# Optimization experiments

Measured on AMD Instinct MI355X. Metric: run time of the kernel, lower is better.

The kernel has to match this reference:

```python
import math
import jax, jax.numpy as jnp
import numpy as np

VMIN, VMAX = 0.0, 1.0
NUM_BINS = 64
SIGMA = 0.5 * (VMAX - VMIN) / NUM_BINS  # matches torch: sigma * (vmax-vmin)/num_bins
EPS = 1e-10


def setup_inputs() -> dict:
    key = jax.random.key(0)
    k1, k2 = jax.random.split(key)
    shape = (2, 1, 96, 96, 96)
    tar = jax.random.uniform(k1, shape, dtype=jnp.float32)
    src = jax.random.uniform(k2, shape, dtype=jnp.float32)
    return {"tar": tar, "src": src}


def _normalise_minmax(x, min_out, max_out):
    # x: (N, P) -- per-sample min-max normalisation to [min_out, max_out]
    xmin = jnp.min(x, axis=1, keepdims=True)
    xmax = jnp.max(x, axis=1, keepdims=True)
    return (x - xmin) / (xmax - xmin + EPS) * (max_out - min_out) + min_out


def _windowed(x, bins):
    # x: (N, P), bins: (B,) -> (N, B, P) Gaussian kernel weights
    d = x[:, None, :] - bins[None, :, None]
    return jnp.exp(-(d * d) / (2.0 * SIGMA * SIGMA)) / math.sqrt(2.0 * math.pi) * SIGMA


def reference(tar, src):
    N = tar.shape[0]
    # use channel 0 only, flatten spatial dims
    t = _normalise_minmax(tar[:, 0].reshape(N, -1), VMIN, VMAX)
    s = _normalise_minmax(src[:, 0].reshape(N, -1), VMIN, VMAX)

    bins = jnp.linspace(VMIN, VMAX, NUM_BINS, dtype=tar.dtype)
    w_tar = _windowed(t, bins)  # (N, B, P)
    w_src = _windowed(s, bins)  # (N, B, P)

    hist_joint = jnp.einsum('nbp,ncp->nbc', w_tar, w_src)  # (N, B, B)
    hist_norm = jnp.sum(hist_joint, axis=(1, 2), keepdims=True)
    p_joint = hist_joint / hist_norm

    p_tar = jnp.sum(p_joint, axis=2)  # (N, B)
    p_src = jnp.sum(p_joint, axis=1)  # (N, B)

    ent_tar = -jnp.sum(p_tar * jnp.log(p_tar + EPS), axis=1)
    ent_src = -jnp.sum(p_src * jnp.log(p_src + EPS), axis=1)
    ent_joint = -jnp.sum(p_joint * jnp.log(p_joint + EPS), axis=(1, 2))

    # normalised=True branch
    return -jnp.mean((ent_tar + ent_src) / ent_joint)
```

## Files before the change

### kernel.cpp

```cpp
#include <hip/hip_runtime.h>
#include <math.h>

#define NBINS 64
#define HIST_ELEMS (NBINS*NBINS)
#define PTS_PER_BLOCK 2304
#define GXN 384
#define CHUNKS 18
#define LSTRIDE 68
#define SQK 1.7256062f
#define SMEM_FLOATS (2*PTS_PER_BLOCK + NBINS*LSTRIDE)
#define RED_BLOCKS 128
#define TILES_PER_WAVE (GXN/4)

typedef float f4 __attribute__((ext_vector_type(4)));
typedef float f2 __attribute__((ext_vector_type(2)));
typedef float f32x4 __attribute__((ext_vector_type(4)));
typedef _Float16 half8 __attribute__((ext_vector_type(8)));
typedef int int4v __attribute__((ext_vector_type(4)));
typedef unsigned int u32x2 __attribute__((ext_vector_type(2)));

static __device__ __forceinline__ half8 pack8(const float* w) {
    int4v v;
    v[0] = __builtin_bit_cast(int, __builtin_amdgcn_cvt_pkrtz(w[0], w[1]));
    v[1] = __builtin_bit_cast(int, __builtin_amdgcn_cvt_pkrtz(w[2], w[3]));
    v[2] = __builtin_bit_cast(int, __builtin_amdgcn_cvt_pkrtz(w[4], w[5]));
    v[3] = __builtin_bit_cast(int, __builtin_amdgcn_cvt_pkrtz(w[6], w[7]));
    return __builtin_bit_cast(half8, v);
}

static __device__ __forceinline__ f2 pk_fma(f2 a, f2 b, f2 c) {
    f2 d;
    asm("v_pk_fma_f32 %0, %1, %2, %3" : "=v"(d) : "v"(a), "v"(b), "v"(c));
    return d;
}
static __device__ __forceinline__ f2 pk_mul(f2 a, f2 b) {
    f2 d;
    asm("v_pk_mul_f32 %0, %1, %2" : "=v"(d) : "v"(a), "v"(b));
    return d;
}

__global__ __launch_bounds__(256) void minmax_kernel(const float* __restrict__ tar,
                                                     const float* __restrict__ src,
                                                     float* __restrict__ pm,
                                                     unsigned* __restrict__ ctr,
                                                     float* __restrict__ hist, int P) {
    const int b = blockIdx.x, n = blockIdx.y, t = blockIdx.z;
    const f4* x = (const f4*)((t == 0 ? tar : src) + (size_t)n * P);
    const int per = (P / 4) / 64;
    float lmin = INFINITY, lmax = -INFINITY;
    for (int i = b * per + threadIdx.x; i < (b + 1) * per; i += 256) {
        f4 v = x[i];
        lmin = fminf(lmin, fminf(fminf(v[0], v[1]), fminf(v[2], v[3])));
        lmax = fmaxf(lmax, fmaxf(fmaxf(v[0], v[1]), fmaxf(v[2], v[3])));
    }
    for (int off = 32; off > 0; off >>= 1) {
        lmin = fminf(lmin, __shfl_down(lmin, off, 64));
        lmax = fmaxf(lmax, __shfl_down(lmax, off, 64));
    }
    __shared__ float smin[4], smax[4];
    const int lane = threadIdx.x & 63, wave = threadIdx.x >> 6;
    if (lane == 0) { smin[wave] = lmin; smax[wave] = lmax; }
    __syncthreads();
    if (threadIdx.x == 0) {
        pm[(n * 2 + t) * 64 + b] =
            fminf(fminf(smin[0], smin[1]), fminf(smin[2], smin[3]));
        pm[256 + (n * 2 + t) * 64 + b] =
            fmaxf(fmaxf(smax[0], smax[1]), fmaxf(smax[2], smax[3]));
    }
    const int flat = b + 64 * n + 128 * t;
    f4* hz = (f4*)hist + flat * 8;
    const f4 z = {0.f, 0.f, 0.f, 0.f};
    if (threadIdx.x < 8) hz[threadIdx.x] = z;
    if (flat == 0 && threadIdx.x == 0) *ctr = 0u;
}

template <int STAGED>
__global__ __launch_bounds__(256) void mfma_hist_kernel(const float* __restrict__ tar,
                                                        const float* __restrict__ src,
                                                        const float* __restrict__ pm,
                                                        _Float16* __restrict__ bh,
                                                        float* __restrict__ hist,
                                                        int P) {
    const int n = blockIdx.y;
    const int bx = blockIdx.x;
    const int tid = threadIdx.x;
    const int lane = tid & 63, wave = tid >> 6;
    const int mlane = lane & 15, quad = lane >> 4;

    __shared__ float smem[SMEM_FLOATS];
    __shared__ float mmred[4];
    float* su_t = smem;
    float* su_s = smem + PTS_PER_BLOCK;
    float* lh = smem + 2 * PTS_PER_BLOCK;

    if (wave == 0) {
        float a = pm[(n * 2 + 0) * 64 + lane];
        float b = pm[256 + (n * 2 + 0) * 64 + lane];
        float c = pm[(n * 2 + 1) * 64 + lane];
        float d = pm[256 + (n * 2 + 1) * 64 + lane];
        for (int off = 32; off > 0; off >>= 1) {
            a = fminf(a, __shfl_down(a, off, 64));
            b = fmaxf(b, __shfl_down(b, off, 64));
            c = fminf(c, __shfl_down(c, off, 64));
            d = fmaxf(d, __shfl_down(d, off, 64));
        }
        if (lane == 0) { mmred[0] = a; mmred[1] = b; mmred[2] = c; mmred[3] = d; }
    }

    {
        const f4* tg = (const f4*)(tar + (size_t)n * P + (size_t)bx * PTS_PER_BLOCK);
        const f4* sg = (const f4*)(src + (size_t)n * P + (size_t)bx * PTS_PER_BLOCK);
        f4* st4 = (f4*)su_t;
        f4* ss4 = (f4*)su_s;
        #pragma unroll
        for (int k = 0; k < 2; ++k) {
            const int i = tid + k * 256;
            st4[i] = tg[i];
            ss4[i] = sg[i];
        }
        if (tid < 64) {
            const int i = 512 + tid;
            st4[i] = tg[i];
            ss4[i] = sg[i];
        }
    }
    __syncthreads();

    const float tmin = mmred[0], tmax = mmred[1];
    const float smin = mmred[2], smax = mmred[3];
    const float tk = 63.0f / (tmax - tmin + 1e-10f) * SQK;
    const float sk = 63.0f / (smax - smin + 1e-10f) * SQK;
    const f2 tkk = {tk, tk}, skk = {sk, sk};
    f2 tneg[4], sneg[4];
    #pragma unroll
    for (int mt = 0; mt < 4; ++mt) {
        const float b = SQK * (float)(mlane + 16 * mt);
        const float tb_ = tmin * tk + b;
        const float sb_ = smin * sk + b;
        tneg[mt] = {-tb_, -tb_};
        sneg[mt] = {-sb_, -sb_};
    }

    f32x4 acc[4][4];
    #pragma unroll
    for (int a = 0; a < 4; ++a)
        #pragma unroll
        for (int b = 0; b < 4; ++b) acc[a][b] = (f32x4){0.f, 0.f, 0.f, 0.f};

    const int kwbase = wave * (32 * CHUNKS) + quad * 8;
    #pragma unroll 3
    for (int c = 0; c < CHUNKS; ++c) {
        const int kbase = kwbase + c * 32;
        const f4* pt4 = (const f4*)&su_t[kbase];
        const f4* ps4 = (const f4*)&su_s[kbase];
        f4 ta = pt4[0], tb = pt4[1];
        f4 sa = ps4[0], sb = ps4[1];
        f2 tp[4], sp[4];
        tp[0] = {ta[0], ta[1]}; tp[1] = {ta[2], ta[3]};
        tp[2] = {tb[0], tb[1]}; tp[3] = {tb[2], tb[3]};
        sp[0] = {sa[0], sa[1]}; sp[1] = {sa[2], sa[3]};
        sp[2] = {sb[0], sb[1]}; sp[3] = {sb[2], sb[3]};

        half8 af[4], bf[4];
        #pragma unroll
        for (int mt = 0; mt < 4; ++mt) {
            float w[8];
            #pragma unroll
            for (int h = 0; h < 4; ++h) {
                f2 d = pk_fma(tp[h], tkk, tneg[mt]);
                f2 s2 = pk_mul(d, d);
                w[2 * h]     = __builtin_amdgcn_exp2f(-s2[0]);
                w[2 * h + 1] = __builtin_amdgcn_exp2f(-s2[1]);
            }
            af[mt] = pack8(w);
        }
        #pragma unroll
        for (int nt = 0; nt < 4; ++nt) {
            float w[8];
            #pragma unroll
            for (int h = 0; h < 4; ++h) {
                f2 d = pk_fma(sp[h], skk, sneg[nt]);
                f2 s2 = pk_mul(d, d);
                w[2 * h]     = __builtin_amdgcn_exp2f(-s2[0]);
                w[2 * h + 1] = __builtin_amdgcn_exp2f(-s2[1]);
            }
            bf[nt] = pack8(w);
        }
        #pragma unroll
        for (int mt = 0; mt < 4; ++mt)
            #pragma unroll
            for (int nt = 0; nt < 4; ++nt)
                acc[mt][nt] = __builtin_amdgcn_mfma_f32_16x16x32_f16(
                    af[mt], bf[nt], acc[mt][nt], 0, 0, 0);
    }

    #pragma unroll
    for (int w = 0; w < 4; ++w) {
        if (wave == w) {
            #pragma unroll
            for (int nt = 0; nt < 4; ++nt)
                #pragma unroll
                for (int mt = 0; mt < 4; ++mt) {
                    f4* p = (f4*)&lh[(16 * nt + mlane) * LSTRIDE + 16 * mt + 4 * quad];
                    if (w == 0) {
                        *p = acc[mt][nt];
                    } else {
                        f4 v = *p;
                        v += acc[mt][nt];
                        *p = v;
                    }
                }
        }
        __syncthreads();
    }

    if (STAGED) {
        u32x2* dst = (u32x2*)(bh + ((size_t)n * GXN + bx) * HIST_ELEMS);
        #pragma unroll
        for (int k = 0; k < 4; ++k) {
            const int i4 = tid + k * 256;
            const int c = i4 >> 4, r4 = (i4 & 15) * 4;
            f4 v = *(const f4*)&lh[c * LSTRIDE + r4];
            u32x2 o;
            o[0] = __builtin_bit_cast(unsigned int, __builtin_amdgcn_cvt_pkrtz(v[0], v[1]));
            o[1] = __builtin_bit_cast(unsigned int, __builtin_amdgcn_cvt_pkrtz(v[2], v[3]));
            dst[i4] = o;
        }
    } else {
        float* gh = hist + (size_t)n * HIST_ELEMS;
        for (int i = tid; i < HIST_ELEMS; i += 256) {
            const int c = i >> 6, r = i & 63;
            unsafeAtomicAdd(&gh[i], lh[c * LSTRIDE + r]);
        }
    }
}

__global__ __launch_bounds__(256) void reduce_finalize_kernel(const _Float16* __restrict__ bh,
                                                              float* __restrict__ hist,
                                                              unsigned* __restrict__ ctr,
                                                              float* __restrict__ out,
                                                              int staged) {
    const int tid = threadIdx.x;
    const int lane = tid & 63, wave = tid >> 6;
    __shared__ float h2[2 * HIST_ELEMS];
    __shared__ float buf[4], rowsum[NBINS], colsum[NBINS], colp[4 * NBINS];
    __shared__ float part[4][64];
    __shared__ int lastflag;

    if (staged) {
        const int g = blockIdx.x * 64 + lane;
        const int n = g >> 12, e = g & 4095;
        const _Float16* p = bh + (((size_t)(n * GXN + wave * TILES_PER_WAVE)) << 12) + e;
        float s = 0.0f;
        #pragma unroll 8
        for (int b = 0; b < TILES_PER_WAVE; ++b) s += (float)p[(size_t)b << 12];
        part[wave][lane] = s;
        __syncthreads();
        if (wave == 0)
            hist[g] = part[0][lane] + part[1][lane] + part[2][lane] + part[3][lane];
    }

    __threadfence();
    if (tid == 0) {
        unsigned old = atomicAdd(ctr, 1u);
        lastflag = (old == RED_BLOCKS - 1) ? 1 : 0;
    }
    __syncthreads();
    if (!lastflag) return;

    for (int i = tid; i < 2 * HIST_ELEMS; i += 256)
        h2[i] = __hip_atomic_load(&hist[i], __ATOMIC_RELAXED, __HIP_MEMORY_SCOPE_SYSTEM);
    __syncthreads();

    float accl = 0.0f;
    for (int nn = 0; nn < 2; ++nn) {
        const float* h = h2 + nn * HIST_ELEMS;
        {
            int r = tid >> 2, q = tid & 3;
            const float* hp = h + r * NBINS + q * 16;
            float sv = 0.0f;
            #pragma unroll
            for (int k = 0; k < 16; ++k) sv += hp[k];
            sv += __shfl_down(sv, 1, 64);
            sv += __shfl_down(sv, 2, 64);
            if (q == 0) rowsum[r] = sv;
        }
        {
            int c = tid & 63, g = tid >> 6;
            const float* hp = h + (g * 16) * NBINS + c;
            float sv = 0.0f;
            #pragma unroll
            for (int k = 0; k < 16; ++k) sv += hp[k * NBINS];
            colp[g * NBINS + c] = sv;
        }
        __syncthreads();
        if (tid < NBINS)
            colsum[tid] = colp[0 * NBINS + tid] + colp[1 * NBINS + tid] +
                          colp[2 * NBINS + tid] + colp[3 * NBINS + tid];
        __syncthreads();

        float tv = (tid < NBINS) ? rowsum[tid] : 0.0f;
        for (int off = 32; off > 0; off >>= 1) tv += __shfl_down(tv, off, 64);
        __syncthreads();
        if (lane == 0) buf[wave] = tv;
        __syncthreads();
        const float total = buf[0] + buf[1] + buf[2] + buf[3];
        const float inv = 1.0f / total;

        float ej = 0.0f;
        for (int i = tid; i < HIST_ELEMS; i += 256) {
            float p = h[i] * inv;
            ej += p * __logf(p + 1e-10f);
        }
        for (int off = 32; off > 0; off >>= 1) ej += __shfl_down(ej, off, 64);
        __syncthreads();
        if (lane == 0) buf[wave] = ej;
        __syncthreads();
        const float entj = -(buf[0] + buf[1] + buf[2] + buf[3]);

        float em = 0.0f;
        if (tid < NBINS) {
            float p = rowsum[tid] * inv;
            em = p * __logf(p + 1e-10f);
        } else if (tid < 2 * NBINS) {
            float p = colsum[tid - NBINS] * inv;
            em = p * __logf(p + 1e-10f);
        }
        for (int off = 32; off > 0; off >>= 1) em += __shfl_down(em, off, 64);
        __syncthreads();
        if (lane == 0) buf[wave] = em;
        __syncthreads();
        const float ents = -(buf[0] + buf[1] + buf[2] + buf[3]);

        accl += ents / entj;
        __syncthreads();
    }
    if (tid == 0) out[0] = -0.5f * accl;
}

extern "C" void kernel_launch(void* const* d_in, const int* in_sizes, int n_in,
                              void* d_out, int out_size, void* d_ws, size_t ws_size,
                              hipStream_t stream) {
    const float* tar = (const float*)d_in[0];
    const float* src = (const float*)d_in[1];
    const int N = 2;
    const int P = in_sizes[0] / N;

    float* pm = (float*)d_ws;
    unsigned* ctr = (unsigned*)((char*)d_ws + 2048);
    float* hist = (float*)((char*)d_ws + 4096);
    _Float16* bh = (_Float16*)((char*)d_ws + 36864);
    float* out = (float*)d_out;

    const size_t need = 36864 + (size_t)2 * GXN * HIST_ELEMS * sizeof(_Float16);

    minmax_kernel<<<dim3(64, N, 2), 256, 0, stream>>>(tar, src, pm, ctr, hist, P);
    if (ws_size >= need) {
        mfma_hist_kernel<1><<<dim3(GXN, N), 256, 0, stream>>>(tar, src, pm, bh, hist, P);
        reduce_finalize_kernel<<<RED_BLOCKS, 256, 0, stream>>>(bh, hist, ctr, out, 1);
    } else {
        mfma_hist_kernel<0><<<dim3(GXN, N), 256, 0, stream>>>(tar, src, pm, bh, hist, P);
        reduce_finalize_kernel<<<RED_BLOCKS, 256, 0, stream>>>(bh, hist, ctr, out, 0);
    }
}
```

Baseline: 129.2 us.

## Halve points per block, drop LDS staging, and widen reduction reads

```diff
diff --git a/kernel.cpp b/kernel.cpp
--- a/kernel.cpp
+++ b/kernel.cpp
@@ -3,14 +3,13 @@
 
 #define NBINS 64
 #define HIST_ELEMS (NBINS*NBINS)
-#define PTS_PER_BLOCK 2304
-#define GXN 384
-#define CHUNKS 18
+#define PTS_PER_BLOCK 1152
+#define GXN 768
+#define CHUNKS 9
 #define LSTRIDE 68
 #define SQK 1.7256062f
-#define SMEM_FLOATS (2*PTS_PER_BLOCK + NBINS*LSTRIDE)
+#define MMB 128
 #define RED_BLOCKS 128
-#define TILES_PER_WAVE (GXN/4)
 
 typedef float f4 __attribute__((ext_vector_type(4)));
 typedef float f2 __attribute__((ext_vector_type(2)));
@@ -46,7 +45,7 @@
                                                      float* __restrict__ hist, int P) {
     const int b = blockIdx.x, n = blockIdx.y, t = blockIdx.z;
     const f4* x = (const f4*)((t == 0 ? tar : src) + (size_t)n * P);
-    const int per = (P / 4) / 64;
+    const int per = (P / 4) / MMB;
     float lmin = INFINITY, lmax = -INFINITY;
     for (int i = b * per + threadIdx.x; i < (b + 1) * per; i += 256) {
         f4 v = x[i];
@@ -62,42 +61,41 @@
     if (lane == 0) { smin[wave] = lmin; smax[wave] = lmax; }
     __syncthreads();
     if (threadIdx.x == 0) {
-        pm[(n * 2 + t) * 64 + b] =
+        pm[(n * 2 + t) * MMB + b] =
             fminf(fminf(smin[0], smin[1]), fminf(smin[2], smin[3]));
-        pm[256 + (n * 2 + t) * 64 + b] =
+        pm[512 + (n * 2 + t) * MMB + b] =
             fmaxf(fmaxf(smax[0], smax[1]), fmaxf(smax[2], smax[3]));
     }
-    const int flat = b + 64 * n + 128 * t;
-    f4* hz = (f4*)hist + flat * 8;
+    const int flat = b + MMB * (n * 2 + t);
+    f4* hz = (f4*)hist + flat * 4;
     const f4 z = {0.f, 0.f, 0.f, 0.f};
-    if (threadIdx.x < 8) hz[threadIdx.x] = z;
+    if (threadIdx.x < 4) hz[threadIdx.x] = z;
     if (flat == 0 && threadIdx.x == 0) *ctr = 0u;
 }
 
 template <int STAGED>
-__global__ __launch_bounds__(256) void mfma_hist_kernel(const float* __restrict__ tar,
-                                                        const float* __restrict__ src,
-                                                        const float* __restrict__ pm,
-                                                        _Float16* __restrict__ bh,
-                                                        float* __restrict__ hist,
-                                                        int P) {
+__global__ __launch_bounds__(256, 6) void mfma_hist_kernel(const float* __restrict__ tar,
+                                                           const float* __restrict__ src,
+                                                           const float* __restrict__ pm,
+                                                           _Float16* __restrict__ bh,
+                                                           float* __restrict__ hist,
+                                                           int P) {
     const int n = blockIdx.y;
     const int bx = blockIdx.x;
     const int tid = threadIdx.x;
     const int lane = tid & 63, wave = tid >> 6;
     const int mlane = lane & 15, quad = lane >> 4;
 
-    __shared__ float smem[SMEM_FLOATS];
+    __shared__ float lh[NBINS * LSTRIDE];
     __shared__ float mmred[4];
-    float* su_t = smem;
-    float* su_s = smem + PTS_PER_BLOCK;
-    float* lh = smem + 2 * PTS_PER_BLOCK;
 
     if (wave == 0) {
-        float a = pm[(n * 2 + 0) * 64 + lane];
-        float b = pm[256 + (n * 2 + 0) * 64 + lane];
-        float c = pm[(n * 2 + 1) * 64 + lane];
-        float d = pm[256 + (n * 2 + 1) * 64 + lane];
+        float a = fminf(pm[(n * 2 + 0) * MMB + lane], pm[(n * 2 + 0) * MMB + 64 + lane]);
+        float b = fmaxf(pm[512 + (n * 2 + 0) * MMB + lane],
+                        pm[512 + (n * 2 + 0) * MMB + 64 + lane]);
+        float c = fminf(pm[(n * 2 + 1) * MMB + lane], pm[(n * 2 + 1) * MMB + 64 + lane]);
+        float d = fmaxf(pm[512 + (n * 2 + 1) * MMB + lane],
+                        pm[512 + (n * 2 + 1) * MMB + 64 + lane]);
         for (int off = 32; off > 0; off >>= 1) {
             a = fminf(a, __shfl_down(a, off, 64));
             b = fmaxf(b, __shfl_down(b, off, 64));
@@ -105,24 +103,6 @@
             d = fmaxf(d, __shfl_down(d, off, 64));
         }
         if (lane == 0) { mmred[0] = a; mmred[1] = b; mmred[2] = c; mmred[3] = d; }
-    }
-
-    {
-        const f4* tg = (const f4*)(tar + (size_t)n * P + (size_t)bx * PTS_PER_BLOCK);
-        const f4* sg = (const f4*)(src + (size_t)n * P + (size_t)bx * PTS_PER_BLOCK);
-        f4* st4 = (f4*)su_t;
-        f4* ss4 = (f4*)su_s;
-        #pragma unroll
-        for (int k = 0; k < 2; ++k) {
-            const int i = tid + k * 256;
-            st4[i] = tg[i];
-            ss4[i] = sg[i];
-        }
-        if (tid < 64) {
-            const int i = 512 + tid;
-            st4[i] = tg[i];
-            ss4[i] = sg[i];
-        }
     }
     __syncthreads();
 
@@ -147,12 +127,14 @@
         #pragma unroll
         for (int b = 0; b < 4; ++b) acc[a][b] = (f32x4){0.f, 0.f, 0.f, 0.f};
 
+    const float* tg = tar + (size_t)n * P + (size_t)bx * PTS_PER_BLOCK;
+    const float* sg = src + (size_t)n * P + (size_t)bx * PTS_PER_BLOCK;
     const int kwbase = wave * (32 * CHUNKS) + quad * 8;
     #pragma unroll 3
     for (int c = 0; c < CHUNKS; ++c) {
         const int kbase = kwbase + c * 32;
-        const f4* pt4 = (const f4*)&su_t[kbase];
-        const f4* ps4 = (const f4*)&su_s[kbase];
+        const f4* pt4 = (const f4*)&tg[kbase];
+        const f4* ps4 = (const f4*)&sg[kbase];
         f4 ta = pt4[0], tb = pt4[1];
         f4 sa = ps4[0], sb = ps4[1];
         f2 tp[4], sp[4];
@@ -243,21 +225,33 @@
     const int tid = threadIdx.x;
     const int lane = tid & 63, wave = tid >> 6;
     __shared__ float h2[2 * HIST_ELEMS];
+    __shared__ f2 part[256];
     __shared__ float buf[4], rowsum[NBINS], colsum[NBINS], colp[4 * NBINS];
-    __shared__ float part[4][64];
     __shared__ int lastflag;
 
     if (staged) {
-        const int g = blockIdx.x * 64 + lane;
-        const int n = g >> 12, e = g & 4095;
-        const _Float16* p = bh + (((size_t)(n * GXN + wave * TILES_PER_WAVE)) << 12) + e;
-        float s = 0.0f;
+        const int n = blockIdx.x >> 6;
+        const int colgrp = blockIdx.x & 63;
+        const unsigned* bhu = (const unsigned*)bh;
+        const int c = colgrp * 32 + (tid & 31);
+        const int seg = tid >> 5;
+        const unsigned* p = bhu + ((size_t)(n * GXN + seg * (GXN / 8))) * 2048 + c;
+        float slo = 0.0f, shi = 0.0f;
         #pragma unroll 8
-        for (int b = 0; b < TILES_PER_WAVE; ++b) s += (float)p[(size_t)b << 12];
-        part[wave][lane] = s;
-        __syncthreads();
-        if (wave == 0)
-            hist[g] = part[0][lane] + part[1][lane] + part[2][lane] + part[3][lane];
+        for (int k = 0; k < GXN / 8; ++k) {
+            unsigned v = p[(size_t)k * 2048];
+            union { unsigned u; _Float16 h[2]; } cv; cv.u = v;
+            slo += (float)cv.h[0];
+            shi += (float)cv.h[1];
+        }
+        part[tid] = (f2){slo, shi};
+        __syncthreads();
+        if (tid < 32) {
+            f2 s = part[tid];
+            #pragma unroll
+            for (int j = 1; j < 8; ++j) s += part[tid + 32 * j];
+            *(f2*)&hist[(size_t)n * HIST_ELEMS + (colgrp * 32 + tid) * 2] = s;
+        }
     }
 
     __threadfence();
@@ -347,14 +341,14 @@
     const int P = in_sizes[0] / N;
 
     float* pm = (float*)d_ws;
-    unsigned* ctr = (unsigned*)((char*)d_ws + 2048);
-    float* hist = (float*)((char*)d_ws + 4096);
-    _Float16* bh = (_Float16*)((char*)d_ws + 36864);
+    unsigned* ctr = (unsigned*)((char*)d_ws + 4096);
+    float* hist = (float*)((char*)d_ws + 8192);
+    _Float16* bh = (_Float16*)((char*)d_ws + 40960);
     float* out = (float*)d_out;
 
-    const size_t need = 36864 + (size_t)2 * GXN * HIST_ELEMS * sizeof(_Float16);
-
-    minmax_kernel<<<dim3(64, N, 2), 256, 0, stream>>>(tar, src, pm, ctr, hist, P);
+    const size_t need = 40960 + (size_t)2 * GXN * HIST_ELEMS * sizeof(_Float16);
+
+    minmax_kernel<<<dim3(MMB, N, 2), 256, 0, stream>>>(tar, src, pm, ctr, hist, P);
     if (ws_size >= need) {
         mfma_hist_kernel<1><<<dim3(GXN, N), 256, 0, stream>>>(tar, src, pm, bh, hist, P);
         reduce_finalize_kernel<<<RED_BLOCKS, 256, 0, stream>>>(bh, hist, ctr, out, 1);
```

After: 333.4 us. 158% more time.

## Shrink per-block points, add occupancy hint, restructure weight compute to cut registers

Applied to the files above, without the earlier changes.

```diff
diff --git a/kernel.cpp b/kernel.cpp
--- a/kernel.cpp
+++ b/kernel.cpp
@@ -3,14 +3,13 @@
 
 #define NBINS 64
 #define HIST_ELEMS (NBINS*NBINS)
-#define PTS_PER_BLOCK 2304
-#define GXN 384
-#define CHUNKS 18
+#define PTS_PER_BLOCK 1728
+#define GXN 512
 #define LSTRIDE 68
 #define SQK 1.7256062f
-#define SMEM_FLOATS (2*PTS_PER_BLOCK + NBINS*LSTRIDE)
 #define RED_BLOCKS 128
 #define TILES_PER_WAVE (GXN/4)
+#define SMEM_FLOATS (2*PTS_PER_BLOCK + NBINS*LSTRIDE)
 
 typedef float f4 __attribute__((ext_vector_type(4)));
 typedef float f2 __attribute__((ext_vector_type(2)));
@@ -36,6 +35,11 @@
 static __device__ __forceinline__ f2 pk_mul(f2 a, f2 b) {
     f2 d;
     asm("v_pk_mul_f32 %0, %1, %2" : "=v"(d) : "v"(a), "v"(b));
+    return d;
+}
+static __device__ __forceinline__ f2 pk_add(f2 a, f2 b) {
+    f2 d;
+    asm("v_pk_add_f32 %0, %1, %2" : "=v"(d) : "v"(a), "v"(b));
     return d;
 }
 
@@ -75,12 +79,12 @@
 }
 
 template <int STAGED>
-__global__ __launch_bounds__(256) void mfma_hist_kernel(const float* __restrict__ tar,
-                                                        const float* __restrict__ src,
-                                                        const float* __restrict__ pm,
-                                                        _Float16* __restrict__ bh,
-                                                        float* __restrict__ hist,
-                                                        int P) {
+__global__ __launch_bounds__(256, 4) void mfma_hist_kernel(const float* __restrict__ tar,
+                                                           const float* __restrict__ src,
+                                                           const float* __restrict__ pm,
+                                                           _Float16* __restrict__ bh,
+                                                           float* __restrict__ hist,
+                                                           int P) {
     const int n = blockIdx.y;
     const int bx = blockIdx.x;
     const int tid = threadIdx.x;
@@ -112,14 +116,13 @@
         const f4* sg = (const f4*)(src + (size_t)n * P + (size_t)bx * PTS_PER_BLOCK);
         f4* st4 = (f4*)su_t;
         f4* ss4 = (f4*)su_s;
-        #pragma unroll
-        for (int k = 0; k < 2; ++k) {
-            const int i = tid + k * 256;
+        {
+            const int i = tid;
             st4[i] = tg[i];
             ss4[i] = sg[i];
         }
-        if (tid < 64) {
-            const int i = 512 + tid;
+        if (tid < 176) {
+            const int i = 256 + tid;
             st4[i] = tg[i];
             ss4[i] = sg[i];
         }
@@ -131,14 +134,15 @@
     const float tk = 63.0f / (tmax - tmin + 1e-10f) * SQK;
     const float sk = 63.0f / (smax - smin + 1e-10f) * SQK;
     const f2 tkk = {tk, tk}, skk = {sk, sk};
-    f2 tneg[4], sneg[4];
+    const float tb0 = -(tmin * tk + SQK * (float)mlane);
+    const float sb0 = -(smin * sk + SQK * (float)mlane);
+    const f2 tbase = {tb0, tb0};
+    const f2 sbase = {sb0, sb0};
+    f2 cmv[3];
     #pragma unroll
-    for (int mt = 0; mt < 4; ++mt) {
-        const float b = SQK * (float)(mlane + 16 * mt);
-        const float tb_ = tmin * tk + b;
-        const float sb_ = smin * sk + b;
-        tneg[mt] = {-tb_, -tb_};
-        sneg[mt] = {-sb_, -sb_};
+    for (int m = 0; m < 3; ++m) {
+        const float c = -16.0f * SQK * (float)(m + 1);
+        cmv[m] = {c, c};
     }
 
     f32x4 acc[4][4];
@@ -147,39 +151,32 @@
         #pragma unroll
         for (int b = 0; b < 4; ++b) acc[a][b] = (f32x4){0.f, 0.f, 0.f, 0.f};
 
-    const int kwbase = wave * (32 * CHUNKS) + quad * 8;
-    #pragma unroll 3
-    for (int c = 0; c < CHUNKS; ++c) {
-        const int kbase = kwbase + c * 32;
+    const int wb = (wave < 2) ? wave * 448 : 896 + (wave - 2) * 416;
+    const int nc = (wave < 2) ? 14 : 13;
+    #pragma unroll 1
+    for (int c = 0; c < nc; ++c) {
+        const int kbase = wb + c * 32 + quad * 8;
         const f4* pt4 = (const f4*)&su_t[kbase];
         const f4* ps4 = (const f4*)&su_s[kbase];
         f4 ta = pt4[0], tb = pt4[1];
         f4 sa = ps4[0], sb = ps4[1];
-        f2 tp[4], sp[4];
-        tp[0] = {ta[0], ta[1]}; tp[1] = {ta[2], ta[3]};
-        tp[2] = {tb[0], tb[1]}; tp[3] = {tb[2], tb[3]};
-        sp[0] = {sa[0], sa[1]}; sp[1] = {sa[2], sa[3]};
-        sp[2] = {sb[0], sb[1]}; sp[3] = {sb[2], sb[3]};
-
-        half8 af[4], bf[4];
-        #pragma unroll
-        for (int mt = 0; mt < 4; ++mt) {
-            float w[8];
-            #pragma unroll
-            for (int h = 0; h < 4; ++h) {
-                f2 d = pk_fma(tp[h], tkk, tneg[mt]);
-                f2 s2 = pk_mul(d, d);
-                w[2 * h]     = __builtin_amdgcn_exp2f(-s2[0]);
-                w[2 * h + 1] = __builtin_amdgcn_exp2f(-s2[1]);
-            }
-            af[mt] = pack8(w);
-        }
+        f2 et[4], es[4];
+        et[0] = pk_fma((f2){ta[0], ta[1]}, tkk, tbase);
+        et[1] = pk_fma((f2){ta[2], ta[3]}, tkk, tbase);
+        et[2] = pk_fma((f2){tb[0], tb[1]}, tkk, tbase);
+        et[3] = pk_fma((f2){tb[2], tb[3]}, tkk, tbase);
+        es[0] = pk_fma((f2){sa[0], sa[1]}, skk, sbase);
+        es[1] = pk_fma((f2){sa[2], sa[3]}, skk, sbase);
+        es[2] = pk_fma((f2){sb[0], sb[1]}, skk, sbase);
+        es[3] = pk_fma((f2){sb[2], sb[3]}, skk, sbase);
+
+        half8 bf[4];
         #pragma unroll
         for (int nt = 0; nt < 4; ++nt) {
             float w[8];
             #pragma unroll
             for (int h = 0; h < 4; ++h) {
-                f2 d = pk_fma(sp[h], skk, sneg[nt]);
+                f2 d = (nt == 0) ? es[h] : pk_add(es[h], cmv[nt - 1]);
                 f2 s2 = pk_mul(d, d);
                 w[2 * h]     = __builtin_amdgcn_exp2f(-s2[0]);
                 w[2 * h + 1] = __builtin_amdgcn_exp2f(-s2[1]);
@@ -187,11 +184,21 @@
             bf[nt] = pack8(w);
         }
         #pragma unroll
-        for (int mt = 0; mt < 4; ++mt)
+        for (int mt = 0; mt < 4; ++mt) {
+            float w[8];
+            #pragma unroll
+            for (int h = 0; h < 4; ++h) {
+                f2 d = (mt == 0) ? et[h] : pk_add(et[h], cmv[mt - 1]);
+                f2 s2 = pk_mul(d, d);
+                w[2 * h]     = __builtin_amdgcn_exp2f(-s2[0]);
+                w[2 * h + 1] = __builtin_amdgcn_exp2f(-s2[1]);
+            }
+            half8 af = pack8(w);
             #pragma unroll
             for (int nt = 0; nt < 4; ++nt)
                 acc[mt][nt] = __builtin_amdgcn_mfma_f32_16x16x32_f16(
-                    af[mt], bf[nt], acc[mt][nt], 0, 0, 0);
+                    af, bf[nt], acc[mt][nt], 0, 0, 0);
+        }
     }
 
     #pragma unroll
```

New measurement: 132.2 us. 1.02x slower.
